# Performance work log

Hardware: AMD Instinct MI355X
Metric: run time of the kernel (lower is better)

## Reference

```python
import jax, jax.numpy as jnp
import numpy as np

IN_F, OUT_F, EMBED = 128, 64, 32
ALPHA = 0.2  # LeakyReLU negative slope


def setup_inputs() -> dict:
    key = jax.random.key(0)
    ks = jax.random.split(key, 8)
    N = 8192
    inp = {
        "input": jax.random.normal(ks[0], (N, IN_F), dtype=jnp.float32),
        "adj": jax.random.uniform(ks[1], (N, N), dtype=jnp.float32),
        "intent_embeds": jax.random.normal(ks[2], (N, EMBED), dtype=jnp.float32),
        # learned parameters
        "W": jax.random.normal(ks[3], (IN_F, OUT_F), dtype=jnp.float32) * 0.1,
        "a": jax.random.normal(ks[4], (2 * OUT_F, 1), dtype=jnp.float32) * 0.1,
        "intent_w": jax.random.normal(ks[5], (1, 2 * EMBED), dtype=jnp.float32) * 0.1,
        "intent_b": jnp.zeros((1,), dtype=jnp.float32),
        "intent_beta": jnp.asarray(0.1, dtype=jnp.float32),
    }
    return inp


def reference(input, adj, intent_embeds, W, a, intent_w, intent_b, intent_beta):
    # h = X W  -> (N, out)
    h = input @ W
    # spatial score e[i,j] = leakyrelu(a1 . h_i + a2 . h_j)  (decomposed, no NxNx2F tensor)
    a1, a2 = a[:OUT_F, 0], a[OUT_F:, 0]
    e_src = h @ a1  # (N,)
    e_dst = h @ a2  # (N,)
    spatial_e = jax.nn.leaky_relu(e_src[:, None] + e_dst[None, :], negative_slope=ALPHA)
    # intent score: Linear([intent_i; intent_j]) = wi.intent_i + wj.intent_j + b
    wi, wj = intent_w[0, :EMBED], intent_w[0, EMBED:]
    ii = intent_embeds @ wi  # (N,)
    jj = intent_embeds @ wj  # (N,)
    intent_e = ii[:, None] + jj[None, :] + intent_b[0]
    total_e = spatial_e + intent_beta * intent_e
    # NOTE: original code computes zero_vec but never masks with adj -> unmasked softmax
    attention = jax.nn.softmax(total_e, axis=0)  # softmax over dim 0, as in source
    h_prime = attention @ h  # (N, out)
    return jax.nn.elu(h_prime)  # concat=True path
```

## Files before the change

### kernel.cpp

```cpp
#include <hip/hip_runtime.h>
#include <hip/hip_bf16.h>

#define NN 8192
#define INF 128
#define OUTF 64
#define EMB 32
#define LOG2E 1.4426950408889634f
#define ISPLIT 64
#define ICH (NN / ISPLIT)
#define MGUARD 64.0f

typedef __attribute__((ext_vector_type(8))) short bf16x8;
typedef __attribute__((ext_vector_type(4))) float f32x4;

#define OFF_HB   0u
#define OFF_UW   1048576u
#define OFF_E12  1114112u
#define OFF_S    1179648u
#define OFF_PART 1212416u


__global__ __launch_bounds__(256) void k1_h(
    const float* __restrict__ input, const float* __restrict__ Wm,
    const float* __restrict__ av, const float* __restrict__ embeds,
    const float* __restrict__ intw, const float* __restrict__ betap,
    ushort* __restrict__ hB, float2* __restrict__ UW,
    float2* __restrict__ e12, float* __restrict__ S)
{
    __shared__ float hl[16][65];
    const int t    = threadIdx.x;
    const int wid  = t >> 6;
    const int lane = t & 63;
    const int blk  = blockIdx.x;
    const int i0 = blk * 16 + wid * 4;

    if (t < 16) S[blk * 16 + t] = 0.f;

    const float a1 = av[lane];
    const float a2 = av[64 + lane];
    const float* x0 = input + (size_t)i0 * INF;

    float acc0 = 0.f, acc1 = 0.f, acc2 = 0.f, acc3 = 0.f;
#pragma unroll 4
    for (int k = 0; k < INF; k += 4) {
        const float wk0 = Wm[(k + 0) * OUTF + lane];
        const float wk1 = Wm[(k + 1) * OUTF + lane];
        const float wk2 = Wm[(k + 2) * OUTF + lane];
        const float wk3 = Wm[(k + 3) * OUTF + lane];
        const float4 xa = *(const float4*)(x0 + k);
        const float4 xb = *(const float4*)(x0 + INF + k);
        const float4 xc = *(const float4*)(x0 + 2 * INF + k);
        const float4 xd = *(const float4*)(x0 + 3 * INF + k);
        acc0 = fmaf(xa.x, wk0, acc0); acc0 = fmaf(xa.y, wk1, acc0);
        acc0 = fmaf(xa.z, wk2, acc0); acc0 = fmaf(xa.w, wk3, acc0);
        acc1 = fmaf(xb.x, wk0, acc1); acc1 = fmaf(xb.y, wk1, acc1);
        acc1 = fmaf(xb.z, wk2, acc1); acc1 = fmaf(xb.w, wk3, acc1);
        acc2 = fmaf(xc.x, wk0, acc2); acc2 = fmaf(xc.y, wk1, acc2);
        acc2 = fmaf(xc.z, wk2, acc2); acc2 = fmaf(xc.w, wk3, acc2);
        acc3 = fmaf(xd.x, wk0, acc3); acc3 = fmaf(xd.y, wk1, acc3);
        acc3 = fmaf(xd.z, wk2, acc3); acc3 = fmaf(xd.w, wk3, acc3);
    }

    hl[wid * 4 + 0][lane] = acc0;
    hl[wid * 4 + 1][lane] = acc1;
    hl[wid * 4 + 2][lane] = acc2;
    hl[wid * 4 + 3][lane] = acc3;

    float accs[4] = {acc0, acc1, acc2, acc3};
#pragma unroll
    for (int r = 0; r < 4; ++r) {
        float v1 = accs[r] * a1;
        float v2 = accs[r] * a2;
#pragma unroll
        for (int o = 32; o > 0; o >>= 1) {
            v1 += __shfl_xor(v1, o);
            v2 += __shfl_xor(v2, o);
        }
        float p = 0.f;
        if (lane < EMB) p = embeds[(size_t)(i0 + r) * EMB + lane] * intw[lane];
#pragma unroll
        for (int o = 16; o > 0; o >>= 1) p += __shfl_xor(p, o);

        if (lane == 0) {
            const float q = betap[0] * p;
            UW[i0 + r] = make_float2(
                __builtin_amdgcn_exp2f((v1 + q) * LOG2E),
                __builtin_amdgcn_exp2f((0.2f * v1 + q) * LOG2E));
            e12[i0 + r] = make_float2(v2 * LOG2E, 0.2f * v2 * LOG2E);
        }
    }

    __syncthreads();
    if (t < 128) {
        const int rr = t >> 6;
        const int of = t & 63;
        const int nb = of >> 4;
        const int r2 = of & 15;
        const int tile = blk >> 1;
        const int g = (blk & 1) * 2 + rr;
        const int l = g * 16 + r2;
        union { bf16x8 v; ushort us[8]; } pk;
#pragma unroll
        for (int e = 0; e < 8; ++e) {
            __hip_bfloat16 b = __float2bfloat16(hl[rr * 8 + e][of]);
            pk.us[e] = *(ushort*)&b;
        }
        *(bf16x8*)(hB + (size_t)(((nb * 256 + tile) * 64 + l) * 8)) = pk.v;
    }
}

__global__ __launch_bounds__(256) void k2_colsum(
    const float2* __restrict__ UW, const float2* __restrict__ e12,
    float* __restrict__ S)
{
    const int j0 = blockIdx.x * 256 + threadIdx.x;
    const int j1 = j0 + 4096;
    const float2 ea = e12[j0];
    const float2 eb = e12[j1];
    const float Ma = fmaxf(ea.x, ea.y) + MGUARD;
    const float Mb = fmaxf(eb.x, eb.y) + MGUARD;
    const float Pa = __builtin_amdgcn_exp2f(ea.x - Ma);
    const float Qa = __builtin_amdgcn_exp2f(ea.y - Ma);
    const float Pb = __builtin_amdgcn_exp2f(eb.x - Mb);
    const float Qb = __builtin_amdgcn_exp2f(eb.y - Mb);

    const float* up = (const float*)UW + (size_t)blockIdx.y * ICH * 2;
    float sa = 0.f, sb = 0.f;
#pragma unroll 8
    for (int rr = 0; rr < ICH * 2; rr += 4) {
        const float4 c = *(const float4*)(up + rr);
        sa += fmaxf(c.x * Pa, c.y * Qa);
        sa += fmaxf(c.z * Pa, c.w * Qa);
        sb += fmaxf(c.x * Pb, c.y * Qb);
        sb += fmaxf(c.z * Pb, c.w * Qb);
    }
    unsafeAtomicAdd(&S[j0], sa);
    unsafeAtomicAdd(&S[j1], sb);
}

__global__ __launch_bounds__(256) void k4_mm(
    const float2* __restrict__ UW, const float2* __restrict__ e12,
    const float* __restrict__ S, const ushort* __restrict__ hB,
    float* __restrict__ part, int jch)
{
    __shared__ float2 pq[2048];

    const int wid  = threadIdx.x >> 6;
    const int lane = threadIdx.x & 63;
    const int r = lane & 15;
    const int g = lane >> 4;
    const int ibase = blockIdx.x * 128 + wid * 32;
    const int jb = blockIdx.y * jch;

    for (int c = threadIdx.x; c < jch; c += 256) {
        const float2 e = e12[jb + c];
        const float M = fmaxf(e.x, e.y) + MGUARD;
        const float inv = 1.0f / S[jb + c];
        pq[c] = make_float2(__builtin_amdgcn_exp2f(e.x - M) * inv,
                            __builtin_amdgcn_exp2f(e.y - M) * inv);
    }
    __syncthreads();

    const float2 c0 = UW[ibase + r];
    const float2 c1 = UW[ibase + 16 + r];

    f32x4 a00 = {0,0,0,0}, a01 = {0,0,0,0}, a02 = {0,0,0,0}, a03 = {0,0,0,0};
    f32x4 a10 = {0,0,0,0}, a11 = {0,0,0,0}, a12 = {0,0,0,0}, a13 = {0,0,0,0};

    for (int j0 = jb; j0 < jb + jch; j0 += 32) {
        const int jj = j0 + g * 8;
        const float* pqp = (const float*)&pq[jj - jb];
        const float4 q0 = *(const float4*)(pqp);
        const float4 q1 = *(const float4*)(pqp + 4);
        const float4 q2 = *(const float4*)(pqp + 8);
        const float4 q3 = *(const float4*)(pqp + 12);

        float e00 = fmaxf(c0.x * q0.x, c0.y * q0.y);
        float e01 = fmaxf(c0.x * q0.z, c0.y * q0.w);
        float e02 = fmaxf(c0.x * q1.x, c0.y * q1.y);
        float e03 = fmaxf(c0.x * q1.z, c0.y * q1.w);
        float e04 = fmaxf(c0.x * q2.x, c0.y * q2.y);
        float e05 = fmaxf(c0.x * q2.z, c0.y * q2.w);
        float e06 = fmaxf(c0.x * q3.x, c0.y * q3.y);
        float e07 = fmaxf(c0.x * q3.z, c0.y * q3.w);

        float e10 = fmaxf(c1.x * q0.x, c1.y * q0.y);
        float e11 = fmaxf(c1.x * q0.z, c1.y * q0.w);
        float e12v= fmaxf(c1.x * q1.x, c1.y * q1.y);
        float e13 = fmaxf(c1.x * q1.z, c1.y * q1.w);
        float e14 = fmaxf(c1.x * q2.x, c1.y * q2.y);
        float e15 = fmaxf(c1.x * q2.z, c1.y * q2.w);
        float e16 = fmaxf(c1.x * q3.x, c1.y * q3.y);
        float e17 = fmaxf(c1.x * q3.z, c1.y * q3.w);

        union { bf16x8 v; unsigned u[4]; } A0, A1;
        asm("v_cvt_pk_bf16_f32 %0, %1, %2" : "=v"(A0.u[0]) : "v"(e00), "v"(e01));
        asm("v_cvt_pk_bf16_f32 %0, %1, %2" : "=v"(A0.u[1]) : "v"(e02), "v"(e03));
        asm("v_cvt_pk_bf16_f32 %0, %1, %2" : "=v"(A0.u[2]) : "v"(e04), "v"(e05));
        asm("v_cvt_pk_bf16_f32 %0, %1, %2" : "=v"(A0.u[3]) : "v"(e06), "v"(e07));
        asm("v_cvt_pk_bf16_f32 %0, %1, %2" : "=v"(A1.u[0]) : "v"(e10), "v"(e11));
        asm("v_cvt_pk_bf16_f32 %0, %1, %2" : "=v"(A1.u[1]) : "v"(e12v),"v"(e13));
        asm("v_cvt_pk_bf16_f32 %0, %1, %2" : "=v"(A1.u[2]) : "v"(e14), "v"(e15));
        asm("v_cvt_pk_bf16_f32 %0, %1, %2" : "=v"(A1.u[3]) : "v"(e16), "v"(e17));

        const int tile = j0 >> 5;
        const ushort* hb = hB + (size_t)(tile * 64 + lane) * 8;
        const bf16x8 b0 = *(const bf16x8*)(hb);
        const bf16x8 b1 = *(const bf16x8*)(hb + 256 * 64 * 8);
        const bf16x8 b2 = *(const bf16x8*)(hb + 2 * 256 * 64 * 8);
        const bf16x8 b3 = *(const bf16x8*)(hb + 3 * 256 * 64 * 8);

        a00 = __builtin_amdgcn_mfma_f32_16x16x32_bf16(A0.v, b0, a00, 0, 0, 0);
        a01 = __builtin_amdgcn_mfma_f32_16x16x32_bf16(A0.v, b1, a01, 0, 0, 0);
        a02 = __builtin_amdgcn_mfma_f32_16x16x32_bf16(A0.v, b2, a02, 0, 0, 0);
        a03 = __builtin_amdgcn_mfma_f32_16x16x32_bf16(A0.v, b3, a03, 0, 0, 0);
        a10 = __builtin_amdgcn_mfma_f32_16x16x32_bf16(A1.v, b0, a10, 0, 0, 0);
        a11 = __builtin_amdgcn_mfma_f32_16x16x32_bf16(A1.v, b1, a11, 0, 0, 0);
        a12 = __builtin_amdgcn_mfma_f32_16x16x32_bf16(A1.v, b2, a12, 0, 0, 0);
        a13 = __builtin_amdgcn_mfma_f32_16x16x32_bf16(A1.v, b3, a13, 0, 0, 0);
    }

    float* pout = part + (size_t)blockIdx.y * (NN * OUTF);
#pragma unroll
    for (int m = 0; m < 4; ++m) {
        const int row0 = ibase + g * 4 + m;
        const int row1 = ibase + 16 + g * 4 + m;
        pout[(size_t)row0 * OUTF + 0  + r] = a00[m];
        pout[(size_t)row0 * OUTF + 16 + r] = a01[m];
        pout[(size_t)row0 * OUTF + 32 + r] = a02[m];
        pout[(size_t)row0 * OUTF + 48 + r] = a03[m];
        pout[(size_t)row1 * OUTF + 0  + r] = a10[m];
        pout[(size_t)row1 * OUTF + 16 + r] = a11[m];
        pout[(size_t)row1 * OUTF + 32 + r] = a12[m];
        pout[(size_t)row1 * OUTF + 48 + r] = a13[m];
    }
}

__global__ __launch_bounds__(256) void k5_combine(
    const float* __restrict__ part, float* __restrict__ out, int JS)
{
    const int base = (blockIdx.x * 256 + threadIdx.x) * 4;
    float4 v = make_float4(0.f, 0.f, 0.f, 0.f);
    for (int s = 0; s < JS; ++s) {
        const float4 p = *(const float4*)(part + (size_t)s * (NN * OUTF) + base);
        v.x += p.x; v.y += p.y; v.z += p.z; v.w += p.w;
    }
    float4 o;
    o.x = v.x > 0.f ? v.x : (__builtin_amdgcn_exp2f(v.x * LOG2E) - 1.f);
    o.y = v.y > 0.f ? v.y : (__builtin_amdgcn_exp2f(v.y * LOG2E) - 1.f);
    o.z = v.z > 0.f ? v.z : (__builtin_amdgcn_exp2f(v.z * LOG2E) - 1.f);
    o.w = v.w > 0.f ? v.w : (__builtin_amdgcn_exp2f(v.w * LOG2E) - 1.f);
    *(float4*)(out + base) = o;
}

extern "C" void kernel_launch(void* const* d_in, const int* in_sizes, int n_in,
                              void* d_out, int out_size, void* d_ws, size_t ws_size,
                              hipStream_t stream)
{
    const float* input  = (const float*)d_in[0];
    const float* embeds = (const float*)d_in[2];
    const float* Wm     = (const float*)d_in[3];
    const float* av     = (const float*)d_in[4];
    const float* intw   = (const float*)d_in[5];
    const float* betap  = (const float*)d_in[7];
    float* out = (float*)d_out;

    char* ws = (char*)d_ws;
    ushort* hB  = (ushort*)(ws + OFF_HB);
    float2* UW  = (float2*)(ws + OFF_UW);
    float2* e12 = (float2*)(ws + OFF_E12);
    float* S    = (float*)(ws + OFF_S);
    float* part = (float*)(ws + OFF_PART);

    int JS = 8;
    while (JS > 4 &&
           (size_t)OFF_PART + (size_t)JS * NN * OUTF * sizeof(float) > ws_size)
        JS >>= 1;
    const int jch = NN / JS;

    k1_h<<<NN / 16, 256, 0, stream>>>(input, Wm, av, embeds, intw, betap,
                                      hB, UW, e12, S);
    k2_colsum<<<dim3(NN / 512, ISPLIT), 256, 0, stream>>>(UW, e12, S);
    k4_mm<<<dim3(NN / 128, JS), 256, 0, stream>>>(UW, e12, S, hB, part, jch);
    k5_combine<<<(NN * OUTF) / 1024, 256, 0, stream>>>(part, out, JS);
}
```

Baseline: 56.95 us.

## Fuse split-K partial reduction and ELU into matmul kernel via LDS reduction

Each block now computes 32 output rows over the full j range. Its four waves each take a quarter of j, and their accumulators are reduced through shared memory before ELU is applied and the result written straight to the output. This removes the global partial buffer, its write and read traffic, and the separate combine kernel launch. The cost is that every block recomputes the full 8192-entry pq table (64KB of LDS), which limits occupancy. The grid also changes from 64x8 blocks to 256 blocks.

```diff
diff --git a/kernel.cpp b/kernel.cpp
--- a/kernel.cpp
+++ b/kernel.cpp
@@ -17,7 +17,6 @@
 #define OFF_UW   1048576u
 #define OFF_E12  1114112u
 #define OFF_S    1179648u
-#define OFF_PART 1212416u
 
 
 __global__ __launch_bounds__(256) void k1_h(
@@ -141,35 +140,39 @@
 __global__ __launch_bounds__(256) void k4_mm(
     const float2* __restrict__ UW, const float2* __restrict__ e12,
     const float* __restrict__ S, const ushort* __restrict__ hB,
-    float* __restrict__ part, int jch)
-{
-    __shared__ float2 pq[2048];
-
-    const int wid  = threadIdx.x >> 6;
-    const int lane = threadIdx.x & 63;
+    float* __restrict__ out)
+{
+    __shared__ union {
+        float2 pq[NN];
+        float red[4][32][64];
+    } sm;
+
+    const int t    = threadIdx.x;
+    const int wid  = t >> 6;
+    const int lane = t & 63;
     const int r = lane & 15;
     const int g = lane >> 4;
-    const int ibase = blockIdx.x * 128 + wid * 32;
-    const int jb = blockIdx.y * jch;
-
-    for (int c = threadIdx.x; c < jch; c += 256) {
-        const float2 e = e12[jb + c];
+    const int i0 = blockIdx.x * 32;
+
+    for (int c = t; c < NN; c += 256) {
+        const float2 e = e12[c];
         const float M = fmaxf(e.x, e.y) + MGUARD;
-        const float inv = 1.0f / S[jb + c];
-        pq[c] = make_float2(__builtin_amdgcn_exp2f(e.x - M) * inv,
-                            __builtin_amdgcn_exp2f(e.y - M) * inv);
-    }
-    __syncthreads();
-
-    const float2 c0 = UW[ibase + r];
-    const float2 c1 = UW[ibase + 16 + r];
+        const float inv = 1.0f / S[c];
+        sm.pq[c] = make_float2(__builtin_amdgcn_exp2f(e.x - M) * inv,
+                               __builtin_amdgcn_exp2f(e.y - M) * inv);
+    }
+    __syncthreads();
+
+    const float2 c0 = UW[i0 + r];
+    const float2 c1 = UW[i0 + 16 + r];
+    const int jb = wid * (NN / 4);
 
     f32x4 a00 = {0,0,0,0}, a01 = {0,0,0,0}, a02 = {0,0,0,0}, a03 = {0,0,0,0};
     f32x4 a10 = {0,0,0,0}, a11 = {0,0,0,0}, a12 = {0,0,0,0}, a13 = {0,0,0,0};
 
-    for (int j0 = jb; j0 < jb + jch; j0 += 32) {
+    for (int j0 = jb; j0 < jb + NN / 4; j0 += 32) {
         const int jj = j0 + g * 8;
-        const float* pqp = (const float*)&pq[jj - jb];
+        const float* pqp = (const float*)&sm.pq[jj];
         const float4 q0 = *(const float4*)(pqp);
         const float4 q1 = *(const float4*)(pqp + 4);
         const float4 q2 = *(const float4*)(pqp + 8);
@@ -220,37 +223,45 @@
         a13 = __builtin_amdgcn_mfma_f32_16x16x32_bf16(A1.v, b3, a13, 0, 0, 0);
     }
 
-    float* pout = part + (size_t)blockIdx.y * (NN * OUTF);
+    __syncthreads();
 #pragma unroll
     for (int m = 0; m < 4; ++m) {
-        const int row0 = ibase + g * 4 + m;
-        const int row1 = ibase + 16 + g * 4 + m;
-        pout[(size_t)row0 * OUTF + 0  + r] = a00[m];
-        pout[(size_t)row0 * OUTF + 16 + r] = a01[m];
-        pout[(size_t)row0 * OUTF + 32 + r] = a02[m];
-        pout[(size_t)row0 * OUTF + 48 + r] = a03[m];
-        pout[(size_t)row1 * OUTF + 0  + r] = a10[m];
-        pout[(size_t)row1 * OUTF + 16 + r] = a11[m];
-        pout[(size_t)row1 * OUTF + 32 + r] = a12[m];
-        pout[(size_t)row1 * OUTF + 48 + r] = a13[m];
-    }
-}
-
-__global__ __launch_bounds__(256) void k5_combine(
-    const float* __restrict__ part, float* __restrict__ out, int JS)
-{
-    const int base = (blockIdx.x * 256 + threadIdx.x) * 4;
-    float4 v = make_float4(0.f, 0.f, 0.f, 0.f);
-    for (int s = 0; s < JS; ++s) {
-        const float4 p = *(const float4*)(part + (size_t)s * (NN * OUTF) + base);
-        v.x += p.x; v.y += p.y; v.z += p.z; v.w += p.w;
-    }
-    float4 o;
-    o.x = v.x > 0.f ? v.x : (__builtin_amdgcn_exp2f(v.x * LOG2E) - 1.f);
-    o.y = v.y > 0.f ? v.y : (__builtin_amdgcn_exp2f(v.y * LOG2E) - 1.f);
-    o.z = v.z > 0.f ? v.z : (__builtin_amdgcn_exp2f(v.z * LOG2E) - 1.f);
-    o.w = v.w > 0.f ? v.w : (__builtin_amdgcn_exp2f(v.w * LOG2E) - 1.f);
-    *(float4*)(out + base) = o;
+        const int row0 = g * 4 + m;
+        const int row1 = 16 + g * 4 + m;
+        sm.red[wid][row0][ 0 + r] = a00[m];
+        sm.red[wid][row0][16 + r] = a01[m];
+        sm.red[wid][row0][32 + r] = a02[m];
+        sm.red[wid][row0][48 + r] = a03[m];
+        sm.red[wid][row1][ 0 + r] = a10[m];
+        sm.red[wid][row1][16 + r] = a11[m];
+        sm.red[wid][row1][32 + r] = a12[m];
+        sm.red[wid][row1][48 + r] = a13[m];
+    }
+    __syncthreads();
+
+    const int row = t >> 3;
+    const int cb  = (t & 7) * 8;
+    float4 v0 = make_float4(0.f, 0.f, 0.f, 0.f);
+    float4 v1 = make_float4(0.f, 0.f, 0.f, 0.f);
+#pragma unroll
+    for (int w = 0; w < 4; ++w) {
+        const float4 p0 = *(const float4*)&sm.red[w][row][cb];
+        const float4 p1 = *(const float4*)&sm.red[w][row][cb + 4];
+        v0.x += p0.x; v0.y += p0.y; v0.z += p0.z; v0.w += p0.w;
+        v1.x += p1.x; v1.y += p1.y; v1.z += p1.z; v1.w += p1.w;
+    }
+    float4 o0, o1;
+    o0.x = v0.x > 0.f ? v0.x : (__builtin_amdgcn_exp2f(v0.x * LOG2E) - 1.f);
+    o0.y = v0.y > 0.f ? v0.y : (__builtin_amdgcn_exp2f(v0.y * LOG2E) - 1.f);
+    o0.z = v0.z > 0.f ? v0.z : (__builtin_amdgcn_exp2f(v0.z * LOG2E) - 1.f);
+    o0.w = v0.w > 0.f ? v0.w : (__builtin_amdgcn_exp2f(v0.w * LOG2E) - 1.f);
+    o1.x = v1.x > 0.f ? v1.x : (__builtin_amdgcn_exp2f(v1.x * LOG2E) - 1.f);
+    o1.y = v1.y > 0.f ? v1.y : (__builtin_amdgcn_exp2f(v1.y * LOG2E) - 1.f);
+    o1.z = v1.z > 0.f ? v1.z : (__builtin_amdgcn_exp2f(v1.z * LOG2E) - 1.f);
+    o1.w = v1.w > 0.f ? v1.w : (__builtin_amdgcn_exp2f(v1.w * LOG2E) - 1.f);
+    float* op = out + (size_t)(i0 + row) * OUTF + cb;
+    *(float4*)(op)     = o0;
+    *(float4*)(op + 4) = o1;
 }
 
 extern "C" void kernel_launch(void* const* d_in, const int* in_sizes, int n_in,
@@ -270,17 +281,9 @@
     float2* UW  = (float2*)(ws + OFF_UW);
     float2* e12 = (float2*)(ws + OFF_E12);
     float* S    = (float*)(ws + OFF_S);
-    float* part = (float*)(ws + OFF_PART);
-
-    int JS = 8;
-    while (JS > 4 &&
-           (size_t)OFF_PART + (size_t)JS * NN * OUTF * sizeof(float) > ws_size)
-        JS >>= 1;
-    const int jch = NN / JS;
 
     k1_h<<<NN / 16, 256, 0, stream>>>(input, Wm, av, embeds, intw, betap,
                                       hB, UW, e12, S);
     k2_colsum<<<dim3(NN / 512, ISPLIT), 256, 0, stream>>>(UW, e12, S);
-    k4_mm<<<dim3(NN / 128, JS), 256, 0, stream>>>(UW, e12, S, hB, part, jch);
-    k5_combine<<<(NN * OUTF) / 1024, 256, 0, stream>>>(part, out, JS);
-}
+    k4_mm<<<NN / 32, 256, 0, stream>>>(UW, e12, S, hB, out);
+}
```

Result: slower. 64.32 us (+12.9%).
